# Kernel optimization log

Measured on AMD Instinct MI355X. Metric: run time of the kernel, lower is better.

Reference implementation:

```python
import jax, jax.numpy as jnp
import numpy as np

INV_SCALE = 8.0  # math.sqrt(64) in the original source


def setup_inputs() -> dict:
    key = jax.random.key(0)
    kq, kk, kv = jax.random.split(key, 3)
    B, S, D = 8, 2048, 128
    q1 = jax.random.normal(kq, (B, S, D), dtype=jnp.float32)
    k1 = jax.random.normal(kk, (B, S, D), dtype=jnp.float32)
    v1 = jax.random.normal(kv, (B, S, D), dtype=jnp.float32)
    return {"q1": q1, "k1": k1, "v1": v1}


def reference(q1, k1, v1):
    # qk = q1 @ k1^T over last two dims  -> [B, S, S]
    scaled_qk = jnp.einsum("bsd,btd->bst", q1, k1) / INV_SCALE
    # original computes softmax(scaled_qk) but never uses it (dead code);
    # dropout is applied to scaled_qk and is identity in eval mode.
    out = jnp.einsum("bst,btd->bsd", scaled_qk, v1)  # [B, S, D]
    return out
```

## Files before the change

kernel.cpp:

```cpp
#include <hip/hip_runtime.h>


#define B 8
#define S 2048
#define D 128
#define CH 32
#define SC 64

typedef __attribute__((ext_vector_type(8))) short short8;
typedef __attribute__((ext_vector_type(4))) float f32x4;

static __device__ __forceinline__ short f2bf(float f) {
    union { float f; unsigned u; } x; x.f = f;
    unsigned r = x.u + 0x7FFF + ((x.u >> 16) & 1);
    return (short)(r >> 16);
}
static __device__ __forceinline__ float bf2f(unsigned short s) {
    union { unsigned u; float f; } x; x.u = ((unsigned)s) << 16;
    return x.f;
}

__global__ __launch_bounds__(256) void s1_ktv(
    const float* __restrict__ K, const float* __restrict__ V,
    unsigned short* __restrict__ P)
{
    int blk = blockIdx.x;
    int b = blk >> 5, ch = blk & 31;
    const float* Kb = K + (size_t)b * S * D + (size_t)ch * SC * D;
    const float* Vb = V + (size_t)b * S * D + (size_t)ch * SC * D;

    int tid = threadIdx.x;
    int w = tid >> 6, l = tid & 63;
    int lr = l & 15, lg = l >> 4;
    int dr0 = (w >> 1) * 64;
    int cc0 = (w & 1) * 64;

    f32x4 acc[4][4];
#pragma unroll
    for (int i = 0; i < 4; i++)
#pragma unroll
        for (int j = 0; j < 4; j++) acc[i][j] = (f32x4)0.f;

#pragma unroll
    for (int ks = 0; ks < 2; ++ks) {
        int sb = ks * 32 + lg * 8;
        short8 af[4], bv[4];
#pragma unroll
        for (int fi = 0; fi < 4; ++fi) {
            const float* kp = Kb + (size_t)sb * D + dr0 + fi * 16 + lr;
            short8 t;
#pragma unroll
            for (int i = 0; i < 8; ++i) t[i] = f2bf(kp[(size_t)i * D]);
            af[fi] = t;
        }
#pragma unroll
        for (int fj = 0; fj < 4; ++fj) {
            const float* vp = Vb + (size_t)sb * D + cc0 + fj * 16 + lr;
            short8 t;
#pragma unroll
            for (int i = 0; i < 8; ++i) t[i] = f2bf(vp[(size_t)i * D]);
            bv[fj] = t;
        }
#pragma unroll
        for (int fi = 0; fi < 4; ++fi)
#pragma unroll
            for (int fj = 0; fj < 4; ++fj)
                acc[fi][fj] = __builtin_amdgcn_mfma_f32_16x16x32_bf16(
                    af[fi], bv[fj], acc[fi][fj], 0, 0, 0);
    }

    unsigned short* Pb = P + (size_t)blk * D * D;
#pragma unroll
    for (int fi = 0; fi < 4; ++fi)
#pragma unroll
        for (int fj = 0; fj < 4; ++fj)
#pragma unroll
            for (int j = 0; j < 4; ++j) {
                int row = dr0 + fi * 16 + lg * 4 + j;
                int col = cc0 + fj * 16 + lr;
                Pb[row * D + col] = (unsigned short)f2bf(acc[fi][fj][j]);
            }
}

__global__ __launch_bounds__(256) void s2_reduce(
    const unsigned short* __restrict__ P, unsigned short* __restrict__ MT)
{
    int idx = blockIdx.x * 256 + threadIdx.x;
    int i0 = idx * 2;
    int b = i0 >> 14;
    int r = i0 & 16383;
    const unsigned short* Pb = P + ((size_t)b * CH) * D * D;
    float s0 = 0.f, s1 = 0.f;
#pragma unroll
    for (int cc = 0; cc < CH; ++cc) {
        unsigned pair = *(const unsigned*)(Pb + (size_t)cc * D * D + r);
        s0 += bf2f((unsigned short)(pair & 0xFFFF));
        s1 += bf2f((unsigned short)(pair >> 16));
    }
    int k = r >> 7, c = r & 127;
    unsigned short* Mb = MT + (size_t)b * D * D;
    Mb[c * D + k]       = (unsigned short)f2bf(s0 * 0.125f);
    Mb[(c + 1) * D + k] = (unsigned short)f2bf(s1 * 0.125f);
}

__global__ __launch_bounds__(256) void s3_qm(
    const float* __restrict__ Q, const unsigned short* __restrict__ MT,
    float* __restrict__ Out)
{
    int blk = blockIdx.x;
    int b = blk >> 5, rc = blk & 31;
    int tid = threadIdx.x;
    int w = tid >> 6, l = tid & 63;
    int lr = l & 15, lg = l >> 4;
    int r0 = rc * 64 + w * 16;

    const float* Qb = Q + (size_t)b * S * D + (size_t)r0 * D;
    const unsigned short* Mb = MT + (size_t)b * D * D;

    f32x4 acc[8];
#pragma unroll
    for (int j = 0; j < 8; j++) acc[j] = (f32x4)0.f;

#pragma unroll
    for (int ks = 0; ks < 4; ++ks) {
        int k0 = ks * 32 + lg * 8;
        const float* qp = Qb + (size_t)lr * D + k0;
        float4 q0 = *(const float4*)qp;
        float4 q1 = *(const float4*)(qp + 4);
        short8 a;
        a[0] = f2bf(q0.x); a[1] = f2bf(q0.y); a[2] = f2bf(q0.z); a[3] = f2bf(q0.w);
        a[4] = f2bf(q1.x); a[5] = f2bf(q1.y); a[6] = f2bf(q1.z); a[7] = f2bf(q1.w);
#pragma unroll
        for (int fj = 0; fj < 8; ++fj) {
            short8 bb = *(const short8*)(Mb + (size_t)(fj * 16 + lr) * D + k0);
            acc[fj] = __builtin_amdgcn_mfma_f32_16x16x32_bf16(a, bb, acc[fj], 0, 0, 0);
        }
    }

    float* Ob = Out + (size_t)b * S * D + (size_t)r0 * D;
#pragma unroll
    for (int fj = 0; fj < 8; ++fj)
#pragma unroll
        for (int j = 0; j < 4; ++j)
            Ob[(size_t)(lg * 4 + j) * D + fj * 16 + lr] = acc[fj][j];
}

extern "C" void kernel_launch(void* const* d_in, const int* in_sizes, int n_in,
                              void* d_out, int out_size, void* d_ws, size_t ws_size,
                              hipStream_t stream)
{
    const float* q = (const float*)d_in[0];
    const float* k = (const float*)d_in[1];
    const float* v = (const float*)d_in[2];
    float* out = (float*)d_out;

    unsigned short* P  = (unsigned short*)d_ws;
    unsigned short* MT = P + (size_t)B * CH * D * D;

    s1_ktv<<<B * CH, 256, 0, stream>>>(k, v, P);
    s2_reduce<<<(B * D * D / 2) / 256, 256, 0, stream>>>(P, MT);
    s3_qm<<<B * CH, 256, 0, stream>>>(q, MT, out);
}
```

Before: 23.45 us.

## Stage K/V chunks in swizzled LDS, halve chunk size, split Q*M output columns

```diff
diff --git a/kernel.cpp b/kernel.cpp
--- a/kernel.cpp
+++ b/kernel.cpp
@@ -4,8 +4,8 @@
 #define B 8
 #define S 2048
 #define D 128
-#define CH 32
-#define SC 64
+#define CH 64
+#define SC 32
 
 typedef __attribute__((ext_vector_type(8))) short short8;
 typedef __attribute__((ext_vector_type(4))) float f32x4;
@@ -25,15 +25,32 @@
     unsigned short* __restrict__ P)
 {
     int blk = blockIdx.x;
-    int b = blk >> 5, ch = blk & 31;
-    const float* Kb = K + (size_t)b * S * D + (size_t)ch * SC * D;
-    const float* Vb = V + (size_t)b * S * D + (size_t)ch * SC * D;
+    int b = blk >> 6, ch = blk & 63;
+    const float* Kb = K + ((size_t)b * S + (size_t)ch * SC) * D;
+    const float* Vb = V + ((size_t)b * S + (size_t)ch * SC) * D;
+
+    __shared__ float Ks[SC * D];
+    __shared__ float Vs[SC * D];
 
     int tid = threadIdx.x;
+
+#pragma unroll
+    for (int it = 0; it < 4; ++it) {
+        int e = it * 1024 + tid * 4;
+        int s = e >> 7, d = e & 127;
+        int d2 = d ^ (((s >> 3) & 1) << 4);
+        float4 kv = *(const float4*)&Kb[e];
+        float4 vv = *(const float4*)&Vb[e];
+        *(float4*)&Ks[s * D + d2] = kv;
+        *(float4*)&Vs[s * D + d2] = vv;
+    }
+    __syncthreads();
+
     int w = tid >> 6, l = tid & 63;
     int lr = l & 15, lg = l >> 4;
     int dr0 = (w >> 1) * 64;
     int cc0 = (w & 1) * 64;
+    int sw = (lg & 1) << 4;
 
     f32x4 acc[4][4];
 #pragma unroll
@@ -41,33 +58,29 @@
 #pragma unroll
         for (int j = 0; j < 4; j++) acc[i][j] = (f32x4)0.f;
 
+    short8 af[4], bv[4];
 #pragma unroll
-    for (int ks = 0; ks < 2; ++ks) {
-        int sb = ks * 32 + lg * 8;
-        short8 af[4], bv[4];
+    for (int fi = 0; fi < 4; ++fi) {
+        int d = (dr0 + fi * 16 + lr) ^ sw;
+        short8 t;
 #pragma unroll
-        for (int fi = 0; fi < 4; ++fi) {
-            const float* kp = Kb + (size_t)sb * D + dr0 + fi * 16 + lr;
-            short8 t;
+        for (int j = 0; j < 8; ++j) t[j] = f2bf(Ks[(lg * 8 + j) * D + d]);
+        af[fi] = t;
+    }
 #pragma unroll
-            for (int i = 0; i < 8; ++i) t[i] = f2bf(kp[(size_t)i * D]);
-            af[fi] = t;
-        }
+    for (int fj = 0; fj < 4; ++fj) {
+        int c = (cc0 + fj * 16 + lr) ^ sw;
+        short8 t;
 #pragma unroll
-        for (int fj = 0; fj < 4; ++fj) {
-            const float* vp = Vb + (size_t)sb * D + cc0 + fj * 16 + lr;
-            short8 t;
+        for (int j = 0; j < 8; ++j) t[j] = f2bf(Vs[(lg * 8 + j) * D + c]);
+        bv[fj] = t;
+    }
 #pragma unroll
-            for (int i = 0; i < 8; ++i) t[i] = f2bf(vp[(size_t)i * D]);
-            bv[fj] = t;
-        }
+    for (int fi = 0; fi < 4; ++fi)
 #pragma unroll
-        for (int fi = 0; fi < 4; ++fi)
-#pragma unroll
-            for (int fj = 0; fj < 4; ++fj)
-                acc[fi][fj] = __builtin_amdgcn_mfma_f32_16x16x32_bf16(
-                    af[fi], bv[fj], acc[fi][fj], 0, 0, 0);
-    }
+        for (int fj = 0; fj < 4; ++fj)
+            acc[fi][fj] = __builtin_amdgcn_mfma_f32_16x16x32_bf16(
+                af[fi], bv[fj], acc[fi][fj], 0, 0, 0);
 
     unsigned short* Pb = P + (size_t)blk * D * D;
 #pragma unroll
@@ -89,9 +102,9 @@
     int i0 = idx * 2;
     int b = i0 >> 14;
     int r = i0 & 16383;
-    const unsigned short* Pb = P + ((size_t)b * CH) * D * D;
+    const unsigned short* Pb = P + (size_t)(b * CH) * D * D;
     float s0 = 0.f, s1 = 0.f;
-#pragma unroll
+#pragma unroll 8
     for (int cc = 0; cc < CH; ++cc) {
         unsigned pair = *(const unsigned*)(Pb + (size_t)cc * D * D + r);
         s0 += bf2f((unsigned short)(pair & 0xFFFF));
@@ -108,18 +121,19 @@
     float* __restrict__ Out)
 {
     int blk = blockIdx.x;
-    int b = blk >> 5, rc = blk & 31;
+    int b = blk >> 6, t = blk & 63;
     int tid = threadIdx.x;
     int w = tid >> 6, l = tid & 63;
     int lr = l & 15, lg = l >> 4;
-    int r0 = rc * 64 + w * 16;
+    int r0 = t * 32 + (w >> 1) * 16;
+    int c0 = (w & 1) * 64;
 
-    const float* Qb = Q + (size_t)b * S * D + (size_t)r0 * D;
+    const float* Qb = Q + ((size_t)b * S + r0) * D;
     const unsigned short* Mb = MT + (size_t)b * D * D;
 
-    f32x4 acc[8];
+    f32x4 acc[4];
 #pragma unroll
-    for (int j = 0; j < 8; j++) acc[j] = (f32x4)0.f;
+    for (int j = 0; j < 4; j++) acc[j] = (f32x4)0.f;
 
 #pragma unroll
     for (int ks = 0; ks < 4; ++ks) {
@@ -131,18 +145,18 @@
         a[0] = f2bf(q0.x); a[1] = f2bf(q0.y); a[2] = f2bf(q0.z); a[3] = f2bf(q0.w);
         a[4] = f2bf(q1.x); a[5] = f2bf(q1.y); a[6] = f2bf(q1.z); a[7] = f2bf(q1.w);
 #pragma unroll
-        for (int fj = 0; fj < 8; ++fj) {
-            short8 bb = *(const short8*)(Mb + (size_t)(fj * 16 + lr) * D + k0);
+        for (int fj = 0; fj < 4; ++fj) {
+            short8 bb = *(const short8*)(Mb + (size_t)(c0 + fj * 16 + lr) * D + k0);
             acc[fj] = __builtin_amdgcn_mfma_f32_16x16x32_bf16(a, bb, acc[fj], 0, 0, 0);
         }
     }
 
-    float* Ob = Out + (size_t)b * S * D + (size_t)r0 * D;
+    float* Ob = Out + ((size_t)b * S + r0) * D;
 #pragma unroll
-    for (int fj = 0; fj < 8; ++fj)
+    for (int fj = 0; fj < 4; ++fj)
 #pragma unroll
         for (int j = 0; j < 4; ++j)
-            Ob[(size_t)(lg * 4 + j) * D + fj * 16 + lr] = acc[fj][j];
+            Ob[(size_t)(lg * 4 + j) * D + c0 + fj * 16 + lr] = acc[fj][j];
 }
 
 extern "C" void kernel_launch(void* const* d_in, const int* in_sizes, int n_in,
```

Result: slower. 28.71 us (+22.5%).
